# Kernel tuning notes

Hardware: AMD Instinct MI355X
Metric: run time of the kernel (lower is better)

Reference implementation:

```python
import jax, jax.numpy as jnp
import numpy as np


def setup_inputs() -> dict:
    key = jax.random.key(0)
    k1, k2, k3, k4 = jax.random.split(key, 4)
    n = 1000000
    nnz = 18000000
    ncols = 8
    field = jax.random.normal(k1, (n, ncols), dtype=jnp.float32)
    lap_vals = jax.random.normal(k2, (nnz,), dtype=jnp.float32)
    lap_row = jax.random.randint(k3, (nnz,), 0, n, dtype=jnp.int32).astype(jnp.int64)
    lap_col = jax.random.randint(k4, (nnz,), 0, n, dtype=jnp.int32).astype(jnp.int64)
    return {"field": field, "lap_vals": lap_vals, "lap_row": lap_row,
            "lap_col": lap_col, "n_vertices": n}


def reference(field, lap_vals, lap_row, lap_col, n_vertices):
    """Apply sparse Laplacian (COO, duplicates summed) to all field columns at once.

    Equivalent to torch.sparse.mm(L, field) where L = coo(row, col, vals, (n, n)).
    One fused gather-multiply-scatter pass replaces the per-column loop.
    """
    field = field.astype(jnp.float32)
    # gather: [nnz, ncols]
    contrib = lap_vals[:, None] * field[lap_col]
    # scatter-add over rows: [n, ncols]
    out = jax.ops.segment_sum(contrib, lap_row, num_segments=n_vertices)
    return out
```

## Files before the change

kernel.cpp:

```cpp
#include <hip/hip_runtime.h>

#define NCOLS  8
#define BLOCK  256
#define NB     256
#define NBKT   1024
#define LG2RPB 10
#define RPB    1024
#define NCB    32

__device__ __forceinline__ int detect_is64(const void* p) {
    const unsigned* w = (const unsigned*)p;
    int is64 = 1;
    #pragma unroll
    for (int k = 0; k < 16; ++k) is64 &= (w[2 * k + 1] == 0u) ? 1 : 0;
    return is64;
}

__device__ __forceinline__ int load_idx(const void* p, int i, int is64) {
    return is64 ? (int)((const long long*)p)[i] : ((const int*)p)[i];
}

__global__ __launch_bounds__(BLOCK) void k_hist(
    const void* __restrict__ rowp, int nnz, int chunk, unsigned* __restrict__ hist)
{
    __shared__ unsigned h[NBKT];
    const int is64 = detect_is64(rowp);
    for (int i = threadIdx.x; i < NBKT; i += BLOCK) h[i] = 0u;
    __syncthreads();
    const int beg = blockIdx.x * chunk;
    const int end = min(nnz, beg + chunk);
    for (int i = beg + threadIdx.x; i < end; i += BLOCK)
        atomicAdd(&h[load_idx(rowp, i, is64) >> LG2RPB], 1u);
    __syncthreads();
    unsigned* row = hist + (size_t)blockIdx.x * NBKT;
    for (int i = threadIdx.x; i < NBKT; i += BLOCK) row[i] = h[i];
}

__global__ __launch_bounds__(BLOCK) void k_colsum(
    unsigned* __restrict__ hist, unsigned* __restrict__ total)
{
    const int c = blockIdx.x * BLOCK + threadIdx.x;
    if (c >= NBKT) return;
    unsigned run = 0;
    for (int b = 0; b < NB; ++b) {
        unsigned t = hist[(size_t)b * NBKT + c];
        hist[(size_t)b * NBKT + c] = run;
        run += t;
    }
    total[c] = run;
}

__global__ __launch_bounds__(1024) void k_scan(
    const unsigned* __restrict__ total, unsigned* __restrict__ base)
{
    __shared__ unsigned s[NBKT];
    const int t = threadIdx.x;
    const unsigned c = total[t];
    s[t] = c;
    __syncthreads();
    for (int off = 1; off < NBKT; off <<= 1) {
        unsigned v = (t >= off) ? s[t - off] : 0u;
        __syncthreads();
        s[t] += v;
        __syncthreads();
    }
    base[t] = s[t] - c;
    if (t == NBKT - 1) base[NBKT] = s[t];
}

__global__ __launch_bounds__(BLOCK) void k_scatter(
    const float* __restrict__ vals, const void* __restrict__ rowp,
    const void* __restrict__ colp, int nnz, int chunk,
    const unsigned* __restrict__ hist, const unsigned* __restrict__ base,
    uint2* __restrict__ records)
{
    __shared__ unsigned cur[NBKT];
    const int is64 = detect_is64(rowp);
    const unsigned* pref = hist + (size_t)blockIdx.x * NBKT;
    for (int i = threadIdx.x; i < NBKT; i += BLOCK) cur[i] = base[i] + pref[i];
    __syncthreads();
    const int beg = blockIdx.x * chunk;
    const int end = min(nnz, beg + chunk);
    for (int i = beg + threadIdx.x; i < end; i += BLOCK) {
        int r = load_idx(rowp, i, is64);
        int c = load_idx(colp, i, is64);
        float v = vals[i];
        unsigned pos = atomicAdd(&cur[r >> LG2RPB], 1u);
        records[pos] = make_uint2((((unsigned)r & (RPB - 1u)) << 20) | (unsigned)c,
                                  __float_as_uint(v));
    }
}

__global__ __launch_bounds__(BLOCK) void k_accum2(
    const uint2* __restrict__ records, const unsigned* __restrict__ base,
    uint2* __restrict__ scratch2, const float* __restrict__ field,
    float* __restrict__ out, int n, int lg2cpb)
{
    __shared__ float acc[NCOLS * RPB];
    __shared__ unsigned cnt[NCB];
    __shared__ unsigned pref[NCB + 1];
    __shared__ unsigned cur[NCB];

    const int b = blockIdx.x;
    const unsigned beg = base[b], end = base[b + 1];

    for (int i = threadIdx.x; i < NCOLS * RPB; i += BLOCK) acc[i] = 0.f;
    if (threadIdx.x < NCB) cnt[threadIdx.x] = 0u;
    __syncthreads();

    for (unsigned i = beg + threadIdx.x; i < end; i += BLOCK) {
        unsigned cb = (records[i].x & 0xFFFFFu) >> lg2cpb;
        atomicAdd(&cnt[cb], 1u);
    }
    __syncthreads();
    if (threadIdx.x == 0) {
        unsigned run = beg;
        #pragma unroll
        for (int k = 0; k < NCB; ++k) { pref[k] = run; cur[k] = run; run += cnt[k]; }
        pref[NCB] = run;
    }
    __syncthreads();

    for (unsigned i = beg + threadIdx.x; i < end; i += BLOCK) {
        uint2 rec = records[i];
        unsigned cb = (rec.x & 0xFFFFFu) >> lg2cpb;
        unsigned pos = atomicAdd(&cur[cb], 1u);
        scratch2[pos] = rec;
    }
    __threadfence_block();
    __syncthreads();

    for (int k = 0; k < NCB; ++k) {
        const unsigned s0 = pref[k], s1 = pref[k + 1];
        for (unsigned i = s0 + threadIdx.x; i < s1; i += BLOCK) {
            const uint2 rec = scratch2[i];
            const unsigned col = rec.x & 0xFFFFFu;
            const unsigned lr  = rec.x >> 20;
            const float v = __uint_as_float(rec.y);
            const float4* f = (const float4*)(field + (size_t)col * NCOLS);
            const float4 f0 = f[0], f1 = f[1];
            atomicAdd(&acc[0 * RPB + lr], v * f0.x);
            atomicAdd(&acc[1 * RPB + lr], v * f0.y);
            atomicAdd(&acc[2 * RPB + lr], v * f0.z);
            atomicAdd(&acc[3 * RPB + lr], v * f0.w);
            atomicAdd(&acc[4 * RPB + lr], v * f1.x);
            atomicAdd(&acc[5 * RPB + lr], v * f1.y);
            atomicAdd(&acc[6 * RPB + lr], v * f1.z);
            atomicAdd(&acc[7 * RPB + lr], v * f1.w);
        }
    }
    __syncthreads();

    const size_t row0 = (size_t)b * RPB;
    for (int t = threadIdx.x; t < NCOLS * RPB; t += BLOCK) {
        int r = t >> 3, j = t & 7;
        size_t gr = row0 + (size_t)r;
        if (gr < (size_t)n) out[gr * NCOLS + j] = acc[j * RPB + r];
    }
}

__global__ __launch_bounds__(BLOCK) void k_accum1(
    const uint2* __restrict__ records, const unsigned* __restrict__ base,
    const float* __restrict__ field, float* __restrict__ out, int n)
{
    __shared__ float acc[NCOLS * RPB];
    for (int i = threadIdx.x; i < NCOLS * RPB; i += BLOCK) acc[i] = 0.f;
    __syncthreads();
    const int b = blockIdx.x;
    const unsigned beg = base[b], end = base[b + 1];
    for (unsigned i = beg + threadIdx.x; i < end; i += BLOCK) {
        const uint2 rec = records[i];
        const unsigned col = rec.x & 0xFFFFFu;
        const unsigned lr  = rec.x >> 20;
        const float v = __uint_as_float(rec.y);
        const float4* f = (const float4*)(field + (size_t)col * NCOLS);
        const float4 f0 = f[0], f1 = f[1];
        atomicAdd(&acc[0 * RPB + lr], v * f0.x);
        atomicAdd(&acc[1 * RPB + lr], v * f0.y);
        atomicAdd(&acc[2 * RPB + lr], v * f0.z);
        atomicAdd(&acc[3 * RPB + lr], v * f0.w);
        atomicAdd(&acc[4 * RPB + lr], v * f1.x);
        atomicAdd(&acc[5 * RPB + lr], v * f1.y);
        atomicAdd(&acc[6 * RPB + lr], v * f1.z);
        atomicAdd(&acc[7 * RPB + lr], v * f1.w);
    }
    __syncthreads();
    const size_t row0 = (size_t)b * RPB;
    for (int t = threadIdx.x; t < NCOLS * RPB; t += BLOCK) {
        int r = t >> 3, j = t & 7;
        size_t gr = row0 + (size_t)r;
        if (gr < (size_t)n) out[gr * NCOLS + j] = acc[j * RPB + r];
    }
}

__global__ __launch_bounds__(BLOCK) void lap_zero_kernel(float4* __restrict__ out, int n4) {
    int i = blockIdx.x * BLOCK + threadIdx.x;
    if (i < n4) out[i] = make_float4(0.f, 0.f, 0.f, 0.f);
}

__global__ __launch_bounds__(BLOCK) void lap_spmm_atomic(
    const float* __restrict__ vals, const void* __restrict__ rowp,
    const void* __restrict__ colp, const float* __restrict__ field,
    float* __restrict__ out, int nnz)
{
    const int is64 = detect_is64(rowp);
    int i = blockIdx.x * BLOCK + threadIdx.x;
    if (i >= nnz) return;
    float v = vals[i];
    int r = load_idx(rowp, i, is64);
    int c = load_idx(colp, i, is64);
    const float4* f = (const float4*)(field + (size_t)c * NCOLS);
    float4 f0 = f[0], f1 = f[1];
    float* o = out + (size_t)r * NCOLS;
    unsafeAtomicAdd(o + 0, v * f0.x);
    unsafeAtomicAdd(o + 1, v * f0.y);
    unsafeAtomicAdd(o + 2, v * f0.z);
    unsafeAtomicAdd(o + 3, v * f0.w);
    unsafeAtomicAdd(o + 4, v * f1.x);
    unsafeAtomicAdd(o + 5, v * f1.y);
    unsafeAtomicAdd(o + 6, v * f1.z);
    unsafeAtomicAdd(o + 7, v * f1.w);
}

extern "C" void kernel_launch(void* const* d_in, const int* in_sizes, int n_in,
                              void* d_out, int out_size, void* d_ws, size_t ws_size,
                              hipStream_t stream) {
    const float* field = (const float*)d_in[0];
    const float* vals  = (const float*)d_in[1];
    const void*  rowp  = d_in[2];
    const void*  colp  = d_in[3];
    float* out = (float*)d_out;

    const int nnz = in_sizes[1];
    const int n   = out_size / NCOLS;
    char* ws = (char*)d_ws;

    const size_t o_hist  = 0;
    const size_t o_total = o_hist + (size_t)NB * NBKT * 4;
    const size_t o_base  = o_total + (size_t)NBKT * 4;
    const size_t o_rec   = (o_base + (size_t)(NBKT + 1) * 4 + 255) & ~(size_t)255;
    const size_t o_scr2  = o_rec + (size_t)nnz * 8;
    const size_t need1   = o_scr2 + (size_t)nnz * 8;
    const size_t need2   = o_scr2;

    if (n <= NBKT * RPB && n <= (1 << 20) && ws_size >= need2) {
        unsigned* hist  = (unsigned*)(ws + o_hist);
        unsigned* total = (unsigned*)(ws + o_total);
        unsigned* base  = (unsigned*)(ws + o_base);
        uint2*    rec   = (uint2*)(ws + o_rec);
        uint2*    scr2  = (uint2*)(ws + o_scr2);

        const int chunk = (nnz + NB - 1) / NB;

        k_hist<<<NB, BLOCK, 0, stream>>>(rowp, nnz, chunk, hist);
        k_colsum<<<(NBKT + BLOCK - 1) / BLOCK, BLOCK, 0, stream>>>(hist, total);
        k_scan<<<1, NBKT, 0, stream>>>(total, base);
        k_scatter<<<NB, BLOCK, 0, stream>>>(vals, rowp, colp, nnz, chunk, hist, base, rec);

        if (ws_size >= need1) {
            int lg = 0;
            while ((1u << lg) < (unsigned)n) ++lg;
            int lg2cpb = lg > 5 ? lg - 5 : 0;
            k_accum2<<<NBKT, BLOCK, 0, stream>>>(rec, base, scr2, field, out, n, lg2cpb);
        } else {
            k_accum1<<<NBKT, BLOCK, 0, stream>>>(rec, base, field, out, n);
        }
        return;
    }

    const int n4 = out_size / 4;
    lap_zero_kernel<<<(n4 + BLOCK - 1) / BLOCK, BLOCK, 0, stream>>>((float4*)out, n4);
    lap_spmm_atomic<<<(nnz + BLOCK - 1) / BLOCK, BLOCK, 0, stream>>>(
        vals, rowp, colp, field, out, nnz);
}
```

Measured before the change: 1.374 ms.

## Parallelize bucket prefix scan and sort records by column via shared index array

Doubles the number of histogram/scatter blocks and replaces the serial per-bucket column sum with a three-stage chunked scan (partial sums, single-block scan, apply), which folds the global base into the per-block offsets. The accumulate kernel no longer copies full 8-byte records into a second global scratch buffer. Instead it builds a 16-bit index permutation in shared memory, grouped by column bucket, and gathers records through it. This removes a global write and reread of all records. The cost is extra shared memory, which may lower occupancy, and a fallback unsorted path when a bucket exceeds CAP entries.

Measured after the change: 1.360 ms. No clear change (-1.0%).

```diff
diff --git a/kernel.cpp b/kernel.cpp
--- a/kernel.cpp
+++ b/kernel.cpp
@@ -2,11 +2,14 @@
 
 #define NCOLS  8
 #define BLOCK  256
-#define NB     256
+#define NB     512
 #define NBKT   1024
 #define LG2RPB 10
 #define RPB    1024
 #define NCB    32
+#define NCHUNK 16
+#define CB     (NB / NCHUNK)
+#define CAP    23040
 
 __device__ __forceinline__ int detect_is64(const void* p) {
     const unsigned* w = (const unsigned*)p;
@@ -36,48 +39,68 @@
     for (int i = threadIdx.x; i < NBKT; i += BLOCK) row[i] = h[i];
 }
 
-__global__ __launch_bounds__(BLOCK) void k_colsum(
-    unsigned* __restrict__ hist, unsigned* __restrict__ total)
-{
-    const int c = blockIdx.x * BLOCK + threadIdx.x;
-    if (c >= NBKT) return;
-    unsigned run = 0;
-    for (int b = 0; b < NB; ++b) {
-        unsigned t = hist[(size_t)b * NBKT + c];
-        hist[(size_t)b * NBKT + c] = run;
+__global__ __launch_bounds__(BLOCK) void k_partial(
+    const unsigned* __restrict__ hist, unsigned* __restrict__ partial)
+{
+    const int t = blockIdx.x * BLOCK + threadIdx.x;
+    const int c = t >> 10, k = t & (NBKT - 1);
+    unsigned s = 0;
+    #pragma unroll 4
+    for (int j = 0; j < CB; ++j) s += hist[(size_t)(c * CB + j) * NBKT + k];
+    partial[(size_t)c * NBKT + k] = s;
+}
+
+__global__ __launch_bounds__(NBKT) void k_scan(
+    unsigned* __restrict__ partial, unsigned* __restrict__ base)
+{
+    __shared__ unsigned s[NBKT];
+    const int k = threadIdx.x;
+    unsigned tot = 0;
+    #pragma unroll
+    for (int c = 0; c < NCHUNK; ++c) tot += partial[(size_t)c * NBKT + k];
+    s[k] = tot;
+    __syncthreads();
+    for (int off = 1; off < NBKT; off <<= 1) {
+        unsigned v = (k >= off) ? s[k - off] : 0u;
+        __syncthreads();
+        s[k] += v;
+        __syncthreads();
+    }
+    unsigned run = s[k] - tot;
+    base[k] = run;
+    if (k == NBKT - 1) base[NBKT] = s[k];
+    #pragma unroll
+    for (int c = 0; c < NCHUNK; ++c) {
+        unsigned t = partial[(size_t)c * NBKT + k];
+        partial[(size_t)c * NBKT + k] = run;
         run += t;
     }
-    total[c] = run;
-}
-
-__global__ __launch_bounds__(1024) void k_scan(
-    const unsigned* __restrict__ total, unsigned* __restrict__ base)
-{
-    __shared__ unsigned s[NBKT];
-    const int t = threadIdx.x;
-    const unsigned c = total[t];
-    s[t] = c;
-    __syncthreads();
-    for (int off = 1; off < NBKT; off <<= 1) {
-        unsigned v = (t >= off) ? s[t - off] : 0u;
-        __syncthreads();
-        s[t] += v;
-        __syncthreads();
-    }
-    base[t] = s[t] - c;
-    if (t == NBKT - 1) base[NBKT] = s[t];
+}
+
+__global__ __launch_bounds__(BLOCK) void k_apply(
+    unsigned* __restrict__ hist, const unsigned* __restrict__ partial)
+{
+    const int t = blockIdx.x * BLOCK + threadIdx.x;
+    const int c = t >> 10, k = t & (NBKT - 1);
+    unsigned run = partial[(size_t)c * NBKT + k];
+    #pragma unroll 4
+    for (int j = 0; j < CB; ++j) {
+        const size_t idx = (size_t)(c * CB + j) * NBKT + k;
+        unsigned v = hist[idx];
+        hist[idx] = run;
+        run += v;
+    }
 }
 
 __global__ __launch_bounds__(BLOCK) void k_scatter(
     const float* __restrict__ vals, const void* __restrict__ rowp,
     const void* __restrict__ colp, int nnz, int chunk,
-    const unsigned* __restrict__ hist, const unsigned* __restrict__ base,
-    uint2* __restrict__ records)
+    const unsigned* __restrict__ hist, uint2* __restrict__ records)
 {
     __shared__ unsigned cur[NBKT];
     const int is64 = detect_is64(rowp);
-    const unsigned* pref = hist + (size_t)blockIdx.x * NBKT;
-    for (int i = threadIdx.x; i < NBKT; i += BLOCK) cur[i] = base[i] + pref[i];
+    const unsigned* wb = hist + (size_t)blockIdx.x * NBKT;
+    for (int i = threadIdx.x; i < NBKT; i += BLOCK) cur[i] = wb[i];
     __syncthreads();
     const int beg = blockIdx.x * chunk;
     const int end = min(nnz, beg + chunk);
@@ -91,49 +114,42 @@
     }
 }
 
-__global__ __launch_bounds__(BLOCK) void k_accum2(
+__global__ __launch_bounds__(BLOCK) void k_accum3(
     const uint2* __restrict__ records, const unsigned* __restrict__ base,
-    uint2* __restrict__ scratch2, const float* __restrict__ field,
-    float* __restrict__ out, int n, int lg2cpb)
+    const float* __restrict__ field, float* __restrict__ out, int n, int lg2cpb)
 {
     __shared__ float acc[NCOLS * RPB];
+    __shared__ unsigned short sidx[CAP];
     __shared__ unsigned cnt[NCB];
-    __shared__ unsigned pref[NCB + 1];
     __shared__ unsigned cur[NCB];
 
     const int b = blockIdx.x;
     const unsigned beg = base[b], end = base[b + 1];
+    const unsigned m = end - beg;
 
     for (int i = threadIdx.x; i < NCOLS * RPB; i += BLOCK) acc[i] = 0.f;
     if (threadIdx.x < NCB) cnt[threadIdx.x] = 0u;
     __syncthreads();
 
-    for (unsigned i = beg + threadIdx.x; i < end; i += BLOCK) {
-        unsigned cb = (records[i].x & 0xFFFFFu) >> lg2cpb;
-        atomicAdd(&cnt[cb], 1u);
-    }
-    __syncthreads();
-    if (threadIdx.x == 0) {
-        unsigned run = beg;
-        #pragma unroll
-        for (int k = 0; k < NCB; ++k) { pref[k] = run; cur[k] = run; run += cnt[k]; }
-        pref[NCB] = run;
-    }
-    __syncthreads();
-
-    for (unsigned i = beg + threadIdx.x; i < end; i += BLOCK) {
-        uint2 rec = records[i];
-        unsigned cb = (rec.x & 0xFFFFFu) >> lg2cpb;
-        unsigned pos = atomicAdd(&cur[cb], 1u);
-        scratch2[pos] = rec;
-    }
-    __threadfence_block();
-    __syncthreads();
-
-    for (int k = 0; k < NCB; ++k) {
-        const unsigned s0 = pref[k], s1 = pref[k + 1];
-        for (unsigned i = s0 + threadIdx.x; i < s1; i += BLOCK) {
-            const uint2 rec = scratch2[i];
+    if (m <= CAP) {
+        for (unsigned i = threadIdx.x; i < m; i += BLOCK) {
+            unsigned cb = (records[beg + i].x & 0xFFFFFu) >> lg2cpb;
+            atomicAdd(&cnt[cb], 1u);
+        }
+        __syncthreads();
+        if (threadIdx.x == 0) {
+            unsigned run = 0;
+            #pragma unroll
+            for (int k = 0; k < NCB; ++k) { cur[k] = run; run += cnt[k]; }
+        }
+        __syncthreads();
+        for (unsigned i = threadIdx.x; i < m; i += BLOCK) {
+            unsigned cb = (records[beg + i].x & 0xFFFFFu) >> lg2cpb;
+            sidx[atomicAdd(&cur[cb], 1u)] = (unsigned short)i;
+        }
+        __syncthreads();
+        for (unsigned i = threadIdx.x; i < m; i += BLOCK) {
+            const uint2 rec = records[beg + sidx[i]];
             const unsigned col = rec.x & 0xFFFFFu;
             const unsigned lr  = rec.x >> 20;
             const float v = __uint_as_float(rec.y);
@@ -148,43 +164,26 @@
             atomicAdd(&acc[6 * RPB + lr], v * f1.z);
             atomicAdd(&acc[7 * RPB + lr], v * f1.w);
         }
-    }
-    __syncthreads();
-
-    const size_t row0 = (size_t)b * RPB;
-    for (int t = threadIdx.x; t < NCOLS * RPB; t += BLOCK) {
-        int r = t >> 3, j = t & 7;
-        size_t gr = row0 + (size_t)r;
-        if (gr < (size_t)n) out[gr * NCOLS + j] = acc[j * RPB + r];
-    }
-}
-
-__global__ __launch_bounds__(BLOCK) void k_accum1(
-    const uint2* __restrict__ records, const unsigned* __restrict__ base,
-    const float* __restrict__ field, float* __restrict__ out, int n)
-{
-    __shared__ float acc[NCOLS * RPB];
-    for (int i = threadIdx.x; i < NCOLS * RPB; i += BLOCK) acc[i] = 0.f;
-    __syncthreads();
-    const int b = blockIdx.x;
-    const unsigned beg = base[b], end = base[b + 1];
-    for (unsigned i = beg + threadIdx.x; i < end; i += BLOCK) {
-        const uint2 rec = records[i];
-        const unsigned col = rec.x & 0xFFFFFu;
-        const unsigned lr  = rec.x >> 20;
-        const float v = __uint_as_float(rec.y);
-        const float4* f = (const float4*)(field + (size_t)col * NCOLS);
-        const float4 f0 = f[0], f1 = f[1];
-        atomicAdd(&acc[0 * RPB + lr], v * f0.x);
-        atomicAdd(&acc[1 * RPB + lr], v * f0.y);
-        atomicAdd(&acc[2 * RPB + lr], v * f0.z);
-        atomicAdd(&acc[3 * RPB + lr], v * f0.w);
-        atomicAdd(&acc[4 * RPB + lr], v * f1.x);
-        atomicAdd(&acc[5 * RPB + lr], v * f1.y);
-        atomicAdd(&acc[6 * RPB + lr], v * f1.z);
-        atomicAdd(&acc[7 * RPB + lr], v * f1.w);
-    }
-    __syncthreads();
+    } else {
+        for (unsigned i = beg + threadIdx.x; i < end; i += BLOCK) {
+            const uint2 rec = records[i];
+            const unsigned col = rec.x & 0xFFFFFu;
+            const unsigned lr  = rec.x >> 20;
+            const float v = __uint_as_float(rec.y);
+            const float4* f = (const float4*)(field + (size_t)col * NCOLS);
+            const float4 f0 = f[0], f1 = f[1];
+            atomicAdd(&acc[0 * RPB + lr], v * f0.x);
+            atomicAdd(&acc[1 * RPB + lr], v * f0.y);
+            atomicAdd(&acc[2 * RPB + lr], v * f0.z);
+            atomicAdd(&acc[3 * RPB + lr], v * f0.w);
+            atomicAdd(&acc[4 * RPB + lr], v * f1.x);
+            atomicAdd(&acc[5 * RPB + lr], v * f1.y);
+            atomicAdd(&acc[6 * RPB + lr], v * f1.z);
+            atomicAdd(&acc[7 * RPB + lr], v * f1.w);
+        }
+    }
+    __syncthreads();
+
     const size_t row0 = (size_t)b * RPB;
     for (int t = threadIdx.x; t < NCOLS * RPB; t += BLOCK) {
         int r = t >> 3, j = t & 7;
@@ -235,36 +234,30 @@
     const int n   = out_size / NCOLS;
     char* ws = (char*)d_ws;
 
-    const size_t o_hist  = 0;
-    const size_t o_total = o_hist + (size_t)NB * NBKT * 4;
-    const size_t o_base  = o_total + (size_t)NBKT * 4;
-    const size_t o_rec   = (o_base + (size_t)(NBKT + 1) * 4 + 255) & ~(size_t)255;
-    const size_t o_scr2  = o_rec + (size_t)nnz * 8;
-    const size_t need1   = o_scr2 + (size_t)nnz * 8;
-    const size_t need2   = o_scr2;
-
-    if (n <= NBKT * RPB && n <= (1 << 20) && ws_size >= need2) {
-        unsigned* hist  = (unsigned*)(ws + o_hist);
-        unsigned* total = (unsigned*)(ws + o_total);
-        unsigned* base  = (unsigned*)(ws + o_base);
-        uint2*    rec   = (uint2*)(ws + o_rec);
-        uint2*    scr2  = (uint2*)(ws + o_scr2);
+    const size_t o_hist    = 0;
+    const size_t o_partial = o_hist + (size_t)NB * NBKT * 4;
+    const size_t o_base    = o_partial + (size_t)NCHUNK * NBKT * 4;
+    const size_t o_rec     = (o_base + (size_t)(NBKT + 1) * 4 + 255) & ~(size_t)255;
+    const size_t need      = o_rec + (size_t)nnz * 8;
+
+    if (n <= NBKT * RPB && n <= (1 << 20) && ws_size >= need) {
+        unsigned* hist    = (unsigned*)(ws + o_hist);
+        unsigned* partial = (unsigned*)(ws + o_partial);
+        unsigned* base    = (unsigned*)(ws + o_base);
+        uint2*    rec     = (uint2*)(ws + o_rec);
 
         const int chunk = (nnz + NB - 1) / NB;
 
+        int lg = 0;
+        while ((1u << lg) < (unsigned)n) ++lg;
+        const int lg2cpb = lg > 5 ? lg - 5 : 0;
+
         k_hist<<<NB, BLOCK, 0, stream>>>(rowp, nnz, chunk, hist);
-        k_colsum<<<(NBKT + BLOCK - 1) / BLOCK, BLOCK, 0, stream>>>(hist, total);
-        k_scan<<<1, NBKT, 0, stream>>>(total, base);
-        k_scatter<<<NB, BLOCK, 0, stream>>>(vals, rowp, colp, nnz, chunk, hist, base, rec);
-
-        if (ws_size >= need1) {
-            int lg = 0;
-            while ((1u << lg) < (unsigned)n) ++lg;
-            int lg2cpb = lg > 5 ? lg - 5 : 0;
-            k_accum2<<<NBKT, BLOCK, 0, stream>>>(rec, base, scr2, field, out, n, lg2cpb);
-        } else {
-            k_accum1<<<NBKT, BLOCK, 0, stream>>>(rec, base, field, out, n);
-        }
+        k_partial<<<NCHUNK * NBKT / BLOCK, BLOCK, 0, stream>>>(hist, partial);
+        k_scan<<<1, NBKT, 0, stream>>>(partial, base);
+        k_apply<<<NCHUNK * NBKT / BLOCK, BLOCK, 0, stream>>>(hist, partial);
+        k_scatter<<<NB, BLOCK, 0, stream>>>(vals, rowp, colp, nnz, chunk, hist, rec);
+        k_accum3<<<NBKT, BLOCK, 0, stream>>>(rec, base, field, out, n, lg2cpb);
         return;
     }
 
```

## Drop column-bucketed secondary sort and fuse histogram colsum into scan kernel

Applied to the files above, without the earlier changes.

Removes the k_accum2 path, which re-sorted each row bucket's records by column block through a scratch buffer before accumulating. k_accum1 now always does the shared-memory accumulation with direct field gathers. The per-bucket column prefix sum and the global scan are merged into one single-block kernel, saving a launch. This removes a full extra read/write pass over the records, but gives up gather locality on the field array.

Result: no change. 1.390 ms (+1.2%).

```diff
diff --git a/kernel.cpp b/kernel.cpp
--- a/kernel.cpp
+++ b/kernel.cpp
@@ -6,7 +6,6 @@
 #define NBKT   1024
 #define LG2RPB 10
 #define RPB    1024
-#define NCB    32
 
 __device__ __forceinline__ int detect_is64(const void* p) {
     const unsigned* w = (const unsigned*)p;
@@ -36,36 +35,29 @@
     for (int i = threadIdx.x; i < NBKT; i += BLOCK) row[i] = h[i];
 }
 
-__global__ __launch_bounds__(BLOCK) void k_colsum(
-    unsigned* __restrict__ hist, unsigned* __restrict__ total)
+__global__ __launch_bounds__(NBKT) void k_scan(
+    unsigned* __restrict__ hist, unsigned* __restrict__ base)
 {
-    const int c = blockIdx.x * BLOCK + threadIdx.x;
-    if (c >= NBKT) return;
+    __shared__ unsigned s[NBKT];
+    const int k = threadIdx.x;
     unsigned run = 0;
+    #pragma unroll 8
     for (int b = 0; b < NB; ++b) {
-        unsigned t = hist[(size_t)b * NBKT + c];
-        hist[(size_t)b * NBKT + c] = run;
+        const size_t idx = (size_t)b * NBKT + k;
+        unsigned t = hist[idx];
+        hist[idx] = run;
         run += t;
     }
-    total[c] = run;
-}
-
-__global__ __launch_bounds__(1024) void k_scan(
-    const unsigned* __restrict__ total, unsigned* __restrict__ base)
-{
-    __shared__ unsigned s[NBKT];
-    const int t = threadIdx.x;
-    const unsigned c = total[t];
-    s[t] = c;
+    s[k] = run;
     __syncthreads();
     for (int off = 1; off < NBKT; off <<= 1) {
-        unsigned v = (t >= off) ? s[t - off] : 0u;
+        unsigned v = (k >= off) ? s[k - off] : 0u;
         __syncthreads();
-        s[t] += v;
+        s[k] += v;
         __syncthreads();
     }
-    base[t] = s[t] - c;
-    if (t == NBKT - 1) base[NBKT] = s[t];
+    base[k] = s[k] - run;
+    if (k == NBKT - 1) base[NBKT] = s[k];
 }
 
 __global__ __launch_bounds__(BLOCK) void k_scatter(
@@ -88,74 +80,6 @@
         unsigned pos = atomicAdd(&cur[r >> LG2RPB], 1u);
         records[pos] = make_uint2((((unsigned)r & (RPB - 1u)) << 20) | (unsigned)c,
                                   __float_as_uint(v));
-    }
-}
-
-__global__ __launch_bounds__(BLOCK) void k_accum2(
-    const uint2* __restrict__ records, const unsigned* __restrict__ base,
-    uint2* __restrict__ scratch2, const float* __restrict__ field,
-    float* __restrict__ out, int n, int lg2cpb)
-{
-    __shared__ float acc[NCOLS * RPB];
-    __shared__ unsigned cnt[NCB];
-    __shared__ unsigned pref[NCB + 1];
-    __shared__ unsigned cur[NCB];
-
-    const int b = blockIdx.x;
-    const unsigned beg = base[b], end = base[b + 1];
-
-    for (int i = threadIdx.x; i < NCOLS * RPB; i += BLOCK) acc[i] = 0.f;
-    if (threadIdx.x < NCB) cnt[threadIdx.x] = 0u;
-    __syncthreads();
-
-    for (unsigned i = beg + threadIdx.x; i < end; i += BLOCK) {
-        unsigned cb = (records[i].x & 0xFFFFFu) >> lg2cpb;
-        atomicAdd(&cnt[cb], 1u);
-    }
-    __syncthreads();
-    if (threadIdx.x == 0) {
-        unsigned run = beg;
-        #pragma unroll
-        for (int k = 0; k < NCB; ++k) { pref[k] = run; cur[k] = run; run += cnt[k]; }
-        pref[NCB] = run;
-    }
-    __syncthreads();
-
-    for (unsigned i = beg + threadIdx.x; i < end; i += BLOCK) {
-        uint2 rec = records[i];
-        unsigned cb = (rec.x & 0xFFFFFu) >> lg2cpb;
-        unsigned pos = atomicAdd(&cur[cb], 1u);
-        scratch2[pos] = rec;
-    }
-    __threadfence_block();
-    __syncthreads();
-
-    for (int k = 0; k < NCB; ++k) {
-        const unsigned s0 = pref[k], s1 = pref[k + 1];
-        for (unsigned i = s0 + threadIdx.x; i < s1; i += BLOCK) {
-            const uint2 rec = scratch2[i];
-            const unsigned col = rec.x & 0xFFFFFu;
-            const unsigned lr  = rec.x >> 20;
-            const float v = __uint_as_float(rec.y);
-            const float4* f = (const float4*)(field + (size_t)col * NCOLS);
-            const float4 f0 = f[0], f1 = f[1];
-            atomicAdd(&acc[0 * RPB + lr], v * f0.x);
-            atomicAdd(&acc[1 * RPB + lr], v * f0.y);
-            atomicAdd(&acc[2 * RPB + lr], v * f0.z);
-            atomicAdd(&acc[3 * RPB + lr], v * f0.w);
-            atomicAdd(&acc[4 * RPB + lr], v * f1.x);
-            atomicAdd(&acc[5 * RPB + lr], v * f1.y);
-            atomicAdd(&acc[6 * RPB + lr], v * f1.z);
-            atomicAdd(&acc[7 * RPB + lr], v * f1.w);
-        }
-    }
-    __syncthreads();
-
-    const size_t row0 = (size_t)b * RPB;
-    for (int t = threadIdx.x; t < NCOLS * RPB; t += BLOCK) {
-        int r = t >> 3, j = t & 7;
-        size_t gr = row0 + (size_t)r;
-        if (gr < (size_t)n) out[gr * NCOLS + j] = acc[j * RPB + r];
     }
 }
 
@@ -235,36 +159,22 @@
     const int n   = out_size / NCOLS;
     char* ws = (char*)d_ws;
 
-    const size_t o_hist  = 0;
-    const size_t o_total = o_hist + (size_t)NB * NBKT * 4;
-    const size_t o_base  = o_total + (size_t)NBKT * 4;
-    const size_t o_rec   = (o_base + (size_t)(NBKT + 1) * 4 + 255) & ~(size_t)255;
-    const size_t o_scr2  = o_rec + (size_t)nnz * 8;
-    const size_t need1   = o_scr2 + (size_t)nnz * 8;
-    const size_t need2   = o_scr2;
+    const size_t o_hist = 0;
+    const size_t o_base = o_hist + (size_t)NB * NBKT * 4;
+    const size_t o_rec  = (o_base + (size_t)(NBKT + 1) * 4 + 255) & ~(size_t)255;
+    const size_t need   = o_rec + (size_t)nnz * 8;
 
-    if (n <= NBKT * RPB && n <= (1 << 20) && ws_size >= need2) {
-        unsigned* hist  = (unsigned*)(ws + o_hist);
-        unsigned* total = (unsigned*)(ws + o_total);
-        unsigned* base  = (unsigned*)(ws + o_base);
-        uint2*    rec   = (uint2*)(ws + o_rec);
-        uint2*    scr2  = (uint2*)(ws + o_scr2);
+    if (n <= NBKT * RPB && n <= (1 << 20) && ws_size >= need) {
+        unsigned* hist = (unsigned*)(ws + o_hist);
+        unsigned* base = (unsigned*)(ws + o_base);
+        uint2*    rec  = (uint2*)(ws + o_rec);
 
         const int chunk = (nnz + NB - 1) / NB;
 
         k_hist<<<NB, BLOCK, 0, stream>>>(rowp, nnz, chunk, hist);
-        k_colsum<<<(NBKT + BLOCK - 1) / BLOCK, BLOCK, 0, stream>>>(hist, total);
-        k_scan<<<1, NBKT, 0, stream>>>(total, base);
+        k_scan<<<1, NBKT, 0, stream>>>(hist, base);
         k_scatter<<<NB, BLOCK, 0, stream>>>(vals, rowp, colp, nnz, chunk, hist, base, rec);
-
-        if (ws_size >= need1) {
-            int lg = 0;
-            while ((1u << lg) < (unsigned)n) ++lg;
-            int lg2cpb = lg > 5 ? lg - 5 : 0;
-            k_accum2<<<NBKT, BLOCK, 0, stream>>>(rec, base, scr2, field, out, n, lg2cpb);
-        } else {
-            k_accum1<<<NBKT, BLOCK, 0, stream>>>(rec, base, field, out, n);
-        }
+        k_accum1<<<NBKT, BLOCK, 0, stream>>>(rec, base, field, out, n);
         return;
     }
 
```
